# Performance work log

Measured on AMD Instinct MI355X. Metric: run time of the kernel, lower is better.

The kernel has to match this reference:

```python
import jax, jax.numpy as jnp
import numpy as np

# Dimensions: B rollouts, NTOT nodes, D max out-degree (dense padded adjacency),
# H agent hidden dim, T max_steps (rollout runs T+1 steps incl. stop step).
B, NTOT, D, H, T = 4096, 100000, 32, 64, 8
STOP = -1          # recorded action value for 'stop' (STOP_RELATION)
NEG = -1e9         # mask value for invalid edges
MIN_TEMPERATURE = 1e-5
LN_EPS = 1e-5


def setup_inputs() -> dict:
    key = jax.random.key(0)
    ks = jax.random.split(key, 12)
    q_tokens = jax.random.normal(ks[0], (B, H), dtype=jnp.float32)
    nbr_node = jax.random.randint(ks[1], (NTOT, D), 0, NTOT, dtype=jnp.int32)
    start_nodes = jax.random.randint(ks[2], (B,), 0, NTOT, dtype=jnp.int32)
    edge_valid = jax.random.randint(ks[3], (NTOT, D), 0, 2) == 1
    s = 1.0 / np.sqrt(H)
    action_keys = jax.random.normal(ks[4], (NTOT, D, H), dtype=jnp.float32) * s
    W_init = jax.random.normal(ks[5], (H, H), dtype=jnp.float32) * s
    W_h = jax.random.normal(ks[6], (H, H), dtype=jnp.float32) * s
    W_k = jax.random.normal(ks[7], (H, H), dtype=jnp.float32) * s
    ln_gamma = jnp.ones((H + 2,), jnp.float32)
    ln_beta = jnp.zeros((H + 2,), jnp.float32)
    stop_w = jax.random.normal(ks[8], (H + 2,), dtype=jnp.float32) * 0.1
    stop_b = jnp.zeros((), jnp.float32)
    temperature = jnp.asarray(1.0, jnp.float32)
    return {
        'q_tokens': q_tokens, 'nbr_node': nbr_node, 'start_nodes': start_nodes,
        'edge_valid': edge_valid, 'action_keys': action_keys,
        'W_init': W_init, 'W_h': W_h, 'W_k': W_k,
        'ln_gamma': ln_gamma, 'ln_beta': ln_beta,
        'stop_w': stop_w, 'stop_b': stop_b, 'temperature': temperature,
    }


def _layernorm(x, g, b):
    mu = x.mean(-1, keepdims=True)
    xc = x - mu
    var = (xc * xc).mean(-1, keepdims=True)
    return xc * jax.lax.rsqrt(var + LN_EPS) * g + b


def reference(q_tokens, nbr_node, start_nodes, edge_valid, action_keys,
              W_init, W_h, W_k, ln_gamma, ln_beta, stop_w, stop_b, temperature):
    tclamp = jnp.maximum(temperature, MIN_TEMPERATURE)
    hidden0 = jnp.tanh(q_tokens @ W_init)              # agent.initialize_state
    nB = q_tokens.shape[0]

    def step(carry, t):
        hidden, curr, stopped = carry                  # [nB,H], [nB], [nB]
        keys = action_keys[curr]                       # gather: [nB,D,H]
        horizon = t >= T
        valid = edge_valid[curr] & (~stopped)[:, None] & (~horizon)
        scores = jnp.einsum('bh,bdh->bd', hidden, keys)
        has_edge = valid.any(-1)
        step_frac = jnp.full((nB, 1), t.astype(hidden.dtype) / T)
        stop_in = jnp.concatenate(
            [hidden, step_frac, has_edge[:, None].astype(hidden.dtype)], -1)
        stop_logit = _layernorm(stop_in, ln_gamma, ln_beta) @ stop_w + stop_b
        logits = jnp.concatenate(
            [jnp.where(valid, scores, NEG), stop_logit[:, None]], -1) / tclamp
        logp = jax.nn.log_softmax(logits, -1)
        action = jnp.where(stopped, D, jnp.argmax(logits, -1))
        log_pf = jnp.where(stopped, 0.0,
                           jnp.take_along_axis(logp, action[:, None], 1)[:, 0])
        chose_stop = action == D
        a = jnp.minimum(action, D - 1)
        tails = jnp.take_along_axis(nbr_node[curr], a[:, None], 1)[:, 0]
        sel = jnp.take_along_axis(keys, a[:, None, None], 1)[:, 0, :]
        new_hidden = jnp.tanh(hidden @ W_h + sel @ W_k)  # agent state update
        hidden = jnp.where(chose_stop[:, None], hidden, new_hidden)
        act_rec = jnp.where(chose_stop, STOP,
                            curr.astype(jnp.int32) * D + a.astype(jnp.int32))
        curr = jnp.where(chose_stop, curr, tails)
        stopped = stopped | chose_stop
        return (hidden, curr, stopped), (log_pf, act_rec.astype(jnp.int32))

    init = (hidden0, start_nodes, jnp.zeros((nB,), bool))
    _, (lp, ar) = jax.lax.scan(step, init, jnp.arange(T + 1))
    log_pf_steps = lp.T                                 # [nB, T+1]
    actions_seq = ar.T                                  # [nB, T+1]
    log_pf_total = log_pf_steps.sum(1)
    num_moves = (actions_seq != STOP).sum(1)
    return actions_seq, log_pf_total, log_pf_steps, num_moves
```

## Files before the change

### kernel.cpp

```cpp
#include <hip/hip_runtime.h>
#include <math.h>


namespace {
constexpr int Bx = 4096;
constexpr int Dx = 32;
constexpr int Hx = 64;
constexpr int Tx = 8;
constexpr float NEGV   = -1e9f;
constexpr float LN_EPS = 1e-5f;
constexpr float MIN_T  = 1e-5f;
}

__device__ __forceinline__ float wsum(float v) {
#pragma unroll
  for (int m = 32; m >= 1; m >>= 1) v += __shfl_xor(v, m);
  return v;
}
__device__ __forceinline__ float wmax(float v) {
#pragma unroll
  for (int m = 32; m >= 1; m >>= 1) v = fmaxf(v, __shfl_xor(v, m));
  return v;
}
__device__ __forceinline__ float lanebc(float v, int i) {
  return __int_as_float(__builtin_amdgcn_readlane(__float_as_int(v), i));
}

__global__ __launch_bounds__(256, 4) void gflow_rollout(
    const float* __restrict__ q_tokens,
    const int*   __restrict__ nbr_node,
    const int*   __restrict__ start_nodes,
    const int*   __restrict__ edge_valid,
    const float* __restrict__ action_keys,
    const float* __restrict__ W_init,
    const float* __restrict__ W_h,
    const float* __restrict__ W_k,
    const float* __restrict__ ln_gamma,
    const float* __restrict__ ln_beta,
    const float* __restrict__ stop_w,
    const float* __restrict__ stop_b,
    const float* __restrict__ temperature,
    float* __restrict__ out)
{
  __shared__ float Wh_s[Hx * Hx];
  __shared__ float Wk_s[Hx * Hx];

  const int tid   = threadIdx.x;
  const int lane  = tid & 63;
  const int wslot = tid >> 6;
  const int b     = blockIdx.x * 4 + wslot;
  const int d     = lane & 31;
  const int half  = lane >> 5;

  int cur = start_nodes[b];

  float kf[32];
  {
    const float4* kp =
        (const float4*)(action_keys + ((size_t)cur * Dx + d) * Hx + half * 32);
#pragma unroll
    for (int c = 0; c < 8; ++c) ((float4*)kf)[c] = kp[c];
  }
  const int* evn_base = (lane < Dx) ? edge_valid : nbr_node;
  int evnb = evn_base[(size_t)cur * Dx + d];

  {
    const float4* sh = (const float4*)W_h;
    const float4* sk = (const float4*)W_k;
    float4* dh = (float4*)Wh_s;
    float4* dk = (float4*)Wk_s;
#pragma unroll
    for (int i = 0; i < 4; ++i) {
      dh[tid + i * 256] = sh[tid + i * 256];
      dk[tid + i * 256] = sk[tid + i * 256];
    }
  }

  const float g_j  = ln_gamma[lane];
  const float be_j = ln_beta[lane];
  const float w_j  = stop_w[lane];
  const float g64 = ln_gamma[64], g65 = ln_gamma[65];
  const float b64 = ln_beta[64],  b65 = ln_beta[65];
  const float w64 = stop_w[64],   w65 = stop_w[65];
  const float sb  = stop_b[0];
  const float tcl = fmaxf(temperature[0], MIN_T);

  float hid;
  {
    const float qv = q_tokens[b * Hx + lane];
    float acc0 = 0.f;
#pragma unroll
    for (int i = 0; i < Hx; ++i)
      acc0 = fmaf(lanebc(qv, i), W_init[i * Hx + lane], acc0);
    hid = tanhf(acc0);
  }

  __syncthreads();

  float lp_total = 0.f;
  int   nmoves   = 0;
  int   tstop    = Tx;

  float* out_act = out + (size_t)b * (Tx + 1);
  float* out_lps = out + (size_t)Bx * (Tx + 1) + Bx + (size_t)b * (Tx + 1);

  for (int t = 0; t <= Tx; ++t) {
    float score = 0.f;
    if (t < Tx) {
      float part = 0.f;
#pragma unroll
      for (int i = 0; i < 32; ++i) {
        const float hv = __shfl(hid, i, 32);
        part = fmaf(kf[i], hv, part);
      }
      score = part + __shfl_xor(part, 32);
    }

    const bool validd = (lane < Dx) && (evnb != 0) && (t < Tx);
    const unsigned long long vm = __ballot(validd);
    const bool has_edge = (vm != 0ULL);

    const float sf = (float)t / (float)Tx;
    const float he = has_edge ? 1.0f : 0.0f;
    float s1 = hid;
    float s2 = hid * hid;
    if (lane == 0) { s1 += sf; s2 = fmaf(sf, sf, s2); }
    if (lane == 1) { s1 += he; s2 = fmaf(he, he, s2); }
#pragma unroll
    for (int m = 32; m >= 1; m >>= 1) {
      s1 += __shfl_xor(s1, m);
      s2 += __shfl_xor(s2, m);
    }
    const float mu   = s1 / 66.0f;
    const float var  = s2 / 66.0f - mu * mu;
    const float rstd = rsqrtf(var + LN_EPS);
    const float dcj  = hid - mu;
    float contrib = (dcj * rstd * g_j + be_j) * w_j;
    if (lane == 0) contrib += ((sf - mu) * rstd * g64 + b64) * w64;
    if (lane == 1) contrib += ((he - mu) * rstd * g65 + b65) * w65;
    const float stop_logit = wsum(contrib) + sb;

    float lg;
    if (lane < Dx)       lg = (validd ? score : NEGV) / tcl;
    else if (lane == Dx) lg = stop_logit / tcl;
    else                 lg = -INFINITY;
    const float mx = wmax(lg);
    const float ex = (lane <= Dx) ? expf(lg - mx) : 0.f;
    const float se = wsum(ex);
    const unsigned long long am = __ballot(lg == mx);
    const int   action = __ffsll(am) - 1;
    const float lga    = __shfl(lg, action);
    const float lp     = lga - mx - logf(se);

    const bool chose_stop = (action == Dx);
    const int  a = min(action, Dx - 1);

    if (lane == 0) {
      out_act[t] = chose_stop ? -1.0f : (float)(cur * Dx + a);
      out_lps[t] = lp;
    }
    lp_total += lp;

    if (chose_stop) { tstop = t; break; }
    nmoves++;

    const float selv = action_keys[((size_t)cur * Dx + a) * Hx + lane];

    cur = __shfl(evnb, Dx + a);
    if (t + 1 < Tx) {
      const float4* kp =
          (const float4*)(action_keys + ((size_t)cur * Dx + d) * Hx + half * 32);
#pragma unroll
      for (int c = 0; c < 8; ++c) ((float4*)kf)[c] = kp[c];
      evnb = evn_base[(size_t)cur * Dx + d];
    }

    float a1 = 0.f, a2 = 0.f;
#pragma unroll
    for (int i = 0; i < Hx; ++i) {
      a1 = fmaf(lanebc(hid,  i), Wh_s[i * Hx + lane], a1);
      a2 = fmaf(lanebc(selv, i), Wk_s[i * Hx + lane], a2);
    }
    hid = tanhf(a1 + a2);
  }

  if (lane == 0) {
    for (int t = tstop + 1; t <= Tx; ++t) { out_act[t] = -1.0f; out_lps[t] = 0.f; }
    out[(size_t)Bx * (Tx + 1) + b] = lp_total;
    out[(size_t)Bx * (Tx + 1) + Bx + (size_t)Bx * (Tx + 1) + b] = (float)nmoves;
  }
}

extern "C" void kernel_launch(void* const* d_in, const int* in_sizes, int n_in,
                              void* d_out, int out_size, void* d_ws, size_t ws_size,
                              hipStream_t stream) {
  const float* q_tokens    = (const float*)d_in[0];
  const int*   nbr_node    = (const int*)d_in[1];
  const int*   start_nodes = (const int*)d_in[2];
  const int*   edge_valid  = (const int*)d_in[3];
  const float* action_keys = (const float*)d_in[4];
  const float* W_init      = (const float*)d_in[5];
  const float* W_h         = (const float*)d_in[6];
  const float* W_k         = (const float*)d_in[7];
  const float* ln_gamma    = (const float*)d_in[8];
  const float* ln_beta     = (const float*)d_in[9];
  const float* stop_w      = (const float*)d_in[10];
  const float* stop_b      = (const float*)d_in[11];
  const float* temperature = (const float*)d_in[12];
  float* out = (float*)d_out;

  gflow_rollout<<<dim3(Bx / 4), dim3(256), 0, stream>>>(
      q_tokens, nbr_node, start_nodes, edge_valid, action_keys,
      W_init, W_h, W_k, ln_gamma, ln_beta, stop_w, stop_b, temperature, out);
}
```

Measured before the change: 943.7 us.

## Coalesce action-key loads and use DPP reductions and interleaved LDS weights

```diff
diff --git a/kernel.cpp b/kernel.cpp
--- a/kernel.cpp
+++ b/kernel.cpp
@@ -12,18 +12,41 @@
 constexpr float MIN_T  = 1e-5f;
 }
 
-__device__ __forceinline__ float wsum(float v) {
-#pragma unroll
-  for (int m = 32; m >= 1; m >>= 1) v += __shfl_xor(v, m);
-  return v;
-}
-__device__ __forceinline__ float wmax(float v) {
-#pragma unroll
-  for (int m = 32; m >= 1; m >>= 1) v = fmaxf(v, __shfl_xor(v, m));
-  return v;
-}
 __device__ __forceinline__ float lanebc(float v, int i) {
   return __int_as_float(__builtin_amdgcn_readlane(__float_as_int(v), i));
+}
+__device__ __forceinline__ float bperm_f(int addr, float v) {
+  return __int_as_float(__builtin_amdgcn_ds_bpermute(addr, __float_as_int(v)));
+}
+template <int CTRL, int RM, bool BC>
+__device__ __forceinline__ float dpp_mov(float old_, float src) {
+  return __int_as_float(__builtin_amdgcn_update_dpp(
+      __float_as_int(old_), __float_as_int(src), CTRL, RM, 0xF, BC));
+}
+__device__ __forceinline__ float dpp_wsum(float v) {
+  v += dpp_mov<0x111, 0xF, true>(0.f, v);
+  v += dpp_mov<0x112, 0xF, true>(0.f, v);
+  v += dpp_mov<0x114, 0xF, true>(0.f, v);
+  v += dpp_mov<0x118, 0xF, true>(0.f, v);
+  v += dpp_mov<0x142, 0xA, true>(0.f, v);
+  v += dpp_mov<0x143, 0xC, true>(0.f, v);
+  return lanebc(v, 63);
+}
+__device__ __forceinline__ float dpp_wmax(float v) {
+  v = fmaxf(v, dpp_mov<0x111, 0xF, false>(v, v));
+  v = fmaxf(v, dpp_mov<0x112, 0xF, false>(v, v));
+  v = fmaxf(v, dpp_mov<0x114, 0xF, false>(v, v));
+  v = fmaxf(v, dpp_mov<0x118, 0xF, false>(v, v));
+  v = fmaxf(v, dpp_mov<0x142, 0xA, false>(v, v));
+  v = fmaxf(v, dpp_mov<0x143, 0xC, false>(v, v));
+  return lanebc(v, 63);
+}
+__device__ __forceinline__ float dpp_rowsum(float v) {
+  v += dpp_mov<0x111, 0xF, true>(0.f, v);
+  v += dpp_mov<0x112, 0xF, true>(0.f, v);
+  v += dpp_mov<0x114, 0xF, true>(0.f, v);
+  v += dpp_mov<0x118, 0xF, true>(0.f, v);
+  return v;
 }
 
 __global__ __launch_bounds__(256, 4) void gflow_rollout(
@@ -42,24 +65,21 @@
     const float* __restrict__ temperature,
     float* __restrict__ out)
 {
-  __shared__ float Wh_s[Hx * Hx];
-  __shared__ float Wk_s[Hx * Hx];
+  __shared__ __align__(16) float2 P_s[Hx * Hx];
 
   const int tid   = threadIdx.x;
   const int lane  = tid & 63;
   const int wslot = tid >> 6;
   const int b     = blockIdx.x * 4 + wslot;
   const int d     = lane & 31;
-  const int half  = lane >> 5;
 
   int cur = start_nodes[b];
 
-  float kf[32];
+  float4 kf4[8];
   {
-    const float4* kp =
-        (const float4*)(action_keys + ((size_t)cur * Dx + d) * Hx + half * 32);
-#pragma unroll
-    for (int c = 0; c < 8; ++c) ((float4*)kf)[c] = kp[c];
+    const float4* kp = (const float4*)(action_keys + (size_t)cur * (Dx * Hx));
+#pragma unroll
+    for (int c = 0; c < 8; ++c) kf4[c] = kp[c * 64 + lane];
   }
   const int* evn_base = (lane < Dx) ? edge_valid : nbr_node;
   int evnb = evn_base[(size_t)cur * Dx + d];
@@ -67,12 +87,14 @@
   {
     const float4* sh = (const float4*)W_h;
     const float4* sk = (const float4*)W_k;
-    float4* dh = (float4*)Wh_s;
-    float4* dk = (float4*)Wk_s;
 #pragma unroll
     for (int i = 0; i < 4; ++i) {
-      dh[tid + i * 256] = sh[tid + i * 256];
-      dk[tid + i * 256] = sk[tid + i * 256];
+      const int idx = tid + i * 256;
+      const float4 h4 = sh[idx];
+      const float4 k4 = sk[idx];
+      float4* dst = (float4*)(P_s + (size_t)idx * 4);
+      dst[0] = make_float4(h4.x, k4.x, h4.y, k4.y);
+      dst[1] = make_float4(h4.z, k4.z, h4.w, k4.w);
     }
   }
 
@@ -85,6 +107,12 @@
   const float sb  = stop_b[0];
   const float tcl = fmaxf(temperature[0], MIN_T);
 
+  const int aq  = (lane & 15) << 4;
+  const int as_ = ((lane & 3) << 6) + 60;
+  const bool sb0 = (lane & 4)  != 0;
+  const bool sb1 = (lane & 8)  != 0;
+  const bool sb2 = (lane & 16) != 0;
+
   float hid;
   {
     const float qv = q_tokens[b * Hx + lane];
@@ -105,15 +133,30 @@
   float* out_lps = out + (size_t)Bx * (Tx + 1) + Bx + (size_t)b * (Tx + 1);
 
   for (int t = 0; t <= Tx; ++t) {
-    float score = 0.f;
+    float score = NEGV;
     if (t < Tx) {
-      float part = 0.f;
-#pragma unroll
-      for (int i = 0; i < 32; ++i) {
-        const float hv = __shfl(hid, i, 32);
-        part = fmaf(kf[i], hv, part);
-      }
-      score = part + __shfl_xor(part, 32);
+      const float hq0 = bperm_f(aq,      hid);
+      const float hq1 = bperm_f(aq + 4,  hid);
+      const float hq2 = bperm_f(aq + 8,  hid);
+      const float hq3 = bperm_f(aq + 12, hid);
+      float part[8];
+#pragma unroll
+      for (int c = 0; c < 8; ++c)
+        part[c] = fmaf(kf4[c].w, hq3,
+                  fmaf(kf4[c].z, hq2,
+                  fmaf(kf4[c].y, hq1, kf4[c].x * hq0)));
+#pragma unroll
+      for (int c = 0; c < 8; ++c) part[c] = dpp_rowsum(part[c]);
+      float bs[8];
+#pragma unroll
+      for (int c = 0; c < 8; ++c) bs[c] = bperm_f(as_, part[c]);
+      const float t01 = sb0 ? bs[1] : bs[0];
+      const float t23 = sb0 ? bs[3] : bs[2];
+      const float t45 = sb0 ? bs[5] : bs[4];
+      const float t67 = sb0 ? bs[7] : bs[6];
+      const float tA  = sb1 ? t23 : t01;
+      const float tB  = sb1 ? t67 : t45;
+      score = sb2 ? tB : tA;
     }
 
     const bool validd = (lane < Dx) && (evnb != 0) && (t < Tx);
@@ -122,34 +165,29 @@
 
     const float sf = (float)t / (float)Tx;
     const float he = has_edge ? 1.0f : 0.0f;
-    float s1 = hid;
-    float s2 = hid * hid;
-    if (lane == 0) { s1 += sf; s2 = fmaf(sf, sf, s2); }
-    if (lane == 1) { s1 += he; s2 = fmaf(he, he, s2); }
-#pragma unroll
-    for (int m = 32; m >= 1; m >>= 1) {
-      s1 += __shfl_xor(s1, m);
-      s2 += __shfl_xor(s2, m);
-    }
-    const float mu   = s1 / 66.0f;
-    const float var  = s2 / 66.0f - mu * mu;
+    float xs = hid;
+    float xq = hid * hid;
+    if (lane == 0) { xs += sf; xq = fmaf(sf, sf, xq); }
+    if (lane == 1) { xs += he; xq = fmaf(he, he, xq); }
+    const float mu   = dpp_wsum(xs) * (1.0f / 66.0f);
+    const float var  = dpp_wsum(xq) * (1.0f / 66.0f) - mu * mu;
     const float rstd = rsqrtf(var + LN_EPS);
     const float dcj  = hid - mu;
     float contrib = (dcj * rstd * g_j + be_j) * w_j;
     if (lane == 0) contrib += ((sf - mu) * rstd * g64 + b64) * w64;
     if (lane == 1) contrib += ((he - mu) * rstd * g65 + b65) * w65;
-    const float stop_logit = wsum(contrib) + sb;
+    const float stop_logit = dpp_wsum(contrib) + sb;
 
     float lg;
     if (lane < Dx)       lg = (validd ? score : NEGV) / tcl;
     else if (lane == Dx) lg = stop_logit / tcl;
     else                 lg = -INFINITY;
-    const float mx = wmax(lg);
+    const float mx = dpp_wmax(lg);
     const float ex = (lane <= Dx) ? expf(lg - mx) : 0.f;
-    const float se = wsum(ex);
+    const float se = dpp_wsum(ex);
     const unsigned long long am = __ballot(lg == mx);
     const int   action = __ffsll(am) - 1;
-    const float lga    = __shfl(lg, action);
+    const float lga    = lanebc(lg, action);
     const float lp     = lga - mx - logf(se);
 
     const bool chose_stop = (action == Dx);
@@ -166,22 +204,25 @@
 
     const float selv = action_keys[((size_t)cur * Dx + a) * Hx + lane];
 
-    cur = __shfl(evnb, Dx + a);
+    cur = __builtin_amdgcn_readlane(evnb, Dx + a);
     if (t + 1 < Tx) {
-      const float4* kp =
-          (const float4*)(action_keys + ((size_t)cur * Dx + d) * Hx + half * 32);
-#pragma unroll
-      for (int c = 0; c < 8; ++c) ((float4*)kf)[c] = kp[c];
+      const float4* kp = (const float4*)(action_keys + (size_t)cur * (Dx * Hx));
+#pragma unroll
+      for (int c = 0; c < 8; ++c) kf4[c] = kp[c * 64 + lane];
       evnb = evn_base[(size_t)cur * Dx + d];
     }
 
-    float a1 = 0.f, a2 = 0.f;
-#pragma unroll
-    for (int i = 0; i < Hx; ++i) {
-      a1 = fmaf(lanebc(hid,  i), Wh_s[i * Hx + lane], a1);
-      a2 = fmaf(lanebc(selv, i), Wk_s[i * Hx + lane], a2);
-    }
-    hid = tanhf(a1 + a2);
+    float a1 = 0.f, a2 = 0.f, c1 = 0.f, c2 = 0.f;
+#pragma unroll
+    for (int i = 0; i < Hx; i += 2) {
+      const float2 wA = P_s[i * 64 + lane];
+      const float2 wB = P_s[(i + 1) * 64 + lane];
+      a1 = fmaf(lanebc(hid,  i),     wA.x, a1);
+      a2 = fmaf(lanebc(selv, i),     wA.y, a2);
+      c1 = fmaf(lanebc(hid,  i + 1), wB.x, c1);
+      c2 = fmaf(lanebc(selv, i + 1), wB.y, c2);
+    }
+    hid = tanhf((a1 + c1) + (a2 + c2));
   }
 
   if (lane == 0) {
```

New measurement: 937.7 us. About the same (-0.6%).
